# Kernel tuning notes

Measured on AMD Instinct MI355X. Metric: run time of the kernel, lower is better.

Reference implementation:

```python
import jax, jax.numpy as jnp
import numpy as np

FFT_LEN = 256
WIN_LEN = 768
FRM_LEN = 128
PPF_TAP = WIN_LEN // FFT_LEN  # 6
SCALE = -256.0
GROUP_DELAY = 648  # module uses group_delay = -648
B, C, S, T = 8, 2, FFT_LEN // 2 + 1, 4096


def _make_lpf(win_len):
    # firwin(win_len, 0.5, window='hann', scale=False) equivalent
    n = np.arange(win_len, dtype=np.float64)
    w = 0.5 - 0.5 * np.cos(2.0 * np.pi * n / (win_len - 1))
    h = w * np.sinc(0.5 * (n - (win_len - 1) / 2.0))
    return jnp.asarray(h, dtype=jnp.float32)


def setup_inputs() -> dict:
    key = jax.random.key(0)
    k1, k2 = jax.random.split(key)
    spectrum_real = jax.random.normal(k1, (B, C, S, T), dtype=jnp.float32)
    spectrum_imag = jax.random.normal(k2, (B, C, S, T), dtype=jnp.float32)
    lpf_coef = _make_lpf(WIN_LEN)
    return {"spectrum_real": spectrum_real, "spectrum_imag": spectrum_imag, "lpf_coef": lpf_coef}


def reference(spectrum_real, spectrum_imag, lpf_coef):
    # spectrum: (B, C, S, T) complex; per-frame irfft over subbands
    spec = jnp.swapaxes(spectrum_real + 1j * spectrum_imag, -1, -2)  # (B,C,T,S)
    fftout = jnp.fft.irfft(spec, n=FFT_LEN, axis=-1)                 # (B,C,T,FFT_LEN)
    rev = fftout[..., ::-1]                                          # comp_in[fft_len-j-1]
    v = jnp.tile(rev, (1, 1, 1, PPF_TAP)) * lpf_coef                 # (B,C,T,WIN_LEN)
    b, c, t, _ = v.shape
    num_samples = t * FRM_LEN
    # overlap-add: frame t contributes v[t] at offset t*FRM_LEN (shifting buffer recurrence)
    idx = jnp.arange(t)[:, None] * FRM_LEN + jnp.arange(WIN_LEN)[None, :]  # (T, WIN_LEN)
    y = jnp.zeros((b, c, num_samples + WIN_LEN), dtype=v.dtype)
    y = y.at[..., idx].add(v)[..., :num_samples]
    y = y * (FRM_LEN * SCALE)
    # circular shift by group delay, then trim the wrapped tail
    y = jnp.roll(y, -GROUP_DELAY, axis=-1)[..., :-GROUP_DELAY]
    return y
```

## Files before the change

### kernel.cpp

```cpp
#include <hip/hip_runtime.h>
#include <hip/hip_bf16.h>
#include <math.h>

#define NBINS   129
#define NFFT    256
#define WINL    768
#define TFRAMES 4096
#define OUTL    523640
#define SHIFT   648
#define WSEG    26
#define CHUNK   (WSEG * 128)
#define NCHUNK  ((OUTL + CHUNK - 1) / CHUNK)
#define FF      32

#define KDIM    288
#define KROW    296
#define GROW    268
#define WBYTES  (16 * 9 * 64 * 16)
#define GBYTES  ((size_t)16 * TFRAMES * 256 * 2)
#define NSTG    17

typedef __attribute__((ext_vector_type(8))) short bf16x8;
typedef __attribute__((ext_vector_type(4))) float f32x4;

static __device__ __forceinline__ ushort f2bf(float x) {
    union { float f; unsigned u; } v; v.f = x;
    unsigned r = v.u + 0x7FFFu + ((v.u >> 16) & 1u);
    return (ushort)(r >> 16);
}

__global__ void build_w_kernel(ushort* __restrict__ wp)
{
    const int gid  = blockIdx.x * 256 + threadIdx.x;
    const int lane = gid & 63;
    const int mtks = gid >> 6;
    const int ks   = mtks % 9;
    const int mt   = mtks / 9;
    const int m    = mt * 16 + (lane & 15);
    const int kb   = ks * 32 + ((lane >> 4) << 3);

    ushort o[8];
    #pragma unroll
    for (int e = 0; e < 8; ++e) {
        const int kap = kb + e;
        float val = 0.f;
        if (kap < 258) {
            const int k = kap >> 1;
            float s, c;
            sincospif((float)(k * (m + 1)) * (1.0f / 128.0f), &s, &c);
            if (kap & 1)  val = (k >= 1 && k <= 127) ? s * (2.0f / 256.0f) : 0.f;
            else          val = (k == 0 || k == 128) ? c * (1.0f / 256.0f)
                                                     : c * (2.0f / 256.0f);
        }
        o[e] = f2bf(val);
    }
    int4 pk;
    pk.x = o[0] | (o[1] << 16); pk.y = o[2] | (o[3] << 16);
    pk.z = o[4] | (o[5] << 16); pk.w = o[6] | (o[7] << 16);
    ((int4*)wp)[gid] = pk;
}

__global__ __launch_bounds__(256, 4)
void pfb_dft_kernel(const float* __restrict__ gre, const float* __restrict__ gim,
                    const ushort* __restrict__ wp, ushort* __restrict__ Gg)
{
    __shared__ ushort s_bufu[FF * KROW];
    ushort* s_Bu = s_bufu;
    ushort (*s_G)[NFFT] = (ushort (*)[NFFT])s_bufu;

    const int t0  = blockIdx.x * FF;
    const int bc  = blockIdx.y;
    const int tid = threadIdx.x;
    const size_t specBase = (size_t)bc * NBINS * TFRAMES;

    float vr[NSTG], vi[NSTG];
    #pragma unroll
    for (int r = 0; r < NSTG; ++r) {
        const int idx = tid + r * 256;
        float a = 0.f, b = 0.f;
        if (idx < NBINS * FF) {
            const int k = idx >> 5, f = idx & 31;
            const size_t g = specBase + (size_t)k * TFRAMES + (size_t)(t0 + f);
            a = gre[g]; b = gim[g];
        }
        vr[r] = a; vi[r] = b;
    }
    #pragma unroll
    for (int r = 0; r < NSTG; ++r) {
        const int idx = tid + r * 256;
        if (idx < NBINS * FF) {
            const int k = idx >> 5, f = idx & 31;
            __hip_bfloat162 p = __float22bfloat162_rn(make_float2(vr[r], vi[r]));
            *(__hip_bfloat162*)&s_Bu[f * KROW + 2 * k] = p;
        }
    }
    for (int idx = tid; idx < FF * (KROW - 258); idx += 256) {
        const int f = idx / (KROW - 258), r = idx - f * (KROW - 258);
        s_Bu[f * KROW + 258 + r] = 0;
    }
    __syncthreads();

    const int lane = tid & 63;
    const int wid  = tid >> 6;
    const int brow = lane & 15;
    const int kgrp = (lane >> 4) << 3;

    bf16x8 bfrag[2][9];
    #pragma unroll
    for (int nt = 0; nt < 2; ++nt)
        #pragma unroll
        for (int ks = 0; ks < 9; ++ks)
            bfrag[nt][ks] = *(const bf16x8*)&s_Bu[(nt * 16 + brow) * KROW + ks * 32 + kgrp];

    f32x4 acc[4][2];
    #pragma unroll
    for (int mi = 0; mi < 4; ++mi)
        #pragma unroll
        for (int nt = 0; nt < 2; ++nt)
            acc[mi][nt] = (f32x4){0.f, 0.f, 0.f, 0.f};

    #pragma unroll 1
    for (int mi = 0; mi < 4; ++mi) {
        const ushort* wbase = wp + ((size_t)((wid * 4 + mi) * 9) * 64 + lane) * 8;
        #pragma unroll
        for (int ks = 0; ks < 9; ++ks) {
            const bf16x8 aw = *(const bf16x8*)(wbase + ks * 512);
            acc[mi][0] = __builtin_amdgcn_mfma_f32_16x16x32_bf16(aw, bfrag[0][ks], acc[mi][0], 0, 0, 0);
            acc[mi][1] = __builtin_amdgcn_mfma_f32_16x16x32_bf16(aw, bfrag[1][ks], acc[mi][1], 0, 0, 0);
        }
    }
    __syncthreads();

    #pragma unroll
    for (int mi = 0; mi < 4; ++mi) {
        const int m0 = (wid * 4 + mi) * 16 + ((lane >> 4) << 2);
        #pragma unroll
        for (int nt = 0; nt < 2; ++nt) {
            const int f = nt * 16 + brow;
            __hip_bfloat162 lo = __float22bfloat162_rn(make_float2(acc[mi][nt].x, acc[mi][nt].y));
            __hip_bfloat162 hi = __float22bfloat162_rn(make_float2(acc[mi][nt].z, acc[mi][nt].w));
            uint2 pk; pk.x = *(unsigned*)&lo; pk.y = *(unsigned*)&hi;
            *(uint2*)&s_G[f][m0] = pk;
        }
    }
    __syncthreads();

    ushort* gout = Gg + ((size_t)bc * TFRAMES + t0) * NFFT;
    #pragma unroll
    for (int j = 0; j < 4; ++j) {
        const int c   = tid + j * 256;
        const int row = c >> 5;
        const int col = (c & 31) * 8;
        *(bf16x8*)&gout[c * 8] = *(const bf16x8*)&s_G[row][col];
    }
}

__global__ __launch_bounds__(256, 8)
void pfb_oa_kernel(const ushort* __restrict__ Gg, const float* __restrict__ glpf,
                   float* __restrict__ out)
{
    const int tid = threadIdx.x;
    const int bc  = blockIdx.y;
    const int i0  = blockIdx.x * 2048 + tid;

    const int s0 = i0 + SHIFT;
    const int b  = s0 & 127;
    float lw[6];
    #pragma unroll
    for (int p = 0; p < 6; ++p) lw[p] = glpf[(p << 7) + b];

    const ushort* Gb = Gg + (size_t)bc * TFRAMES * NFFT;
    const size_t outBase = (size_t)bc * OUTL;

    #pragma unroll
    for (int j = 0; j < 8; ++j) {
        const int i = i0 + j * 256;
        if (i < OUTL) {
            const int a = (i + SHIFT) >> 7;
            const ushort* gp = Gb + (size_t)a * NFFT + b;
            float sum = 0.f;
            #pragma unroll
            for (int p = 0; p < 6; ++p) {
                union { unsigned u_; float f; } g;
                g.u_ = ((unsigned)gp[-(p << 8) + ((p & 1) << 7)]) << 16;
                sum += lw[p] * g.f;
            }
            out[outBase + i] = sum * (-32768.0f);
        }
    }
}

__global__ __launch_bounds__(256, 4)
void pfb_mfma_kernel(const float* __restrict__ gre, const float* __restrict__ gim,
                     const float* __restrict__ glpf, const ushort* __restrict__ wp,
                     float* __restrict__ out)
{
    __shared__ ushort s_bufu[FF * KROW];
    __shared__ float  s_lpf[WINL];
    ushort* s_Bu = s_bufu;
    ushort (*s_G)[GROW] = (ushort (*)[GROW])s_bufu;

    const int q   = blockIdx.x;
    const int bc  = blockIdx.y;
    const int tid = threadIdx.x;
    const int t0  = WSEG * q;
    const size_t specBase = (size_t)bc * NBINS * TFRAMES;

    for (int idx = tid; idx < WINL; idx += 256) s_lpf[idx] = glpf[idx];

    float vr[NSTG], vi[NSTG];
    #pragma unroll
    for (int r = 0; r < NSTG; ++r) {
        const int idx = tid + r * 256;
        const int k = idx >> 5, f = idx & 31;
        const int t = t0 + f;
        const bool ok = (idx < NBINS * FF) && (t < TFRAMES);
        float a = 0.f, bb = 0.f;
        if (ok) {
            const size_t g = specBase + (size_t)k * TFRAMES + (size_t)t;
            a = gre[g]; bb = gim[g];
        }
        vr[r] = a; vi[r] = bb;
    }
    #pragma unroll
    for (int r = 0; r < NSTG; ++r) {
        const int idx = tid + r * 256;
        if (idx < NBINS * FF) {
            const int k = idx >> 5, f = idx & 31;
            __hip_bfloat162 p = __float22bfloat162_rn(make_float2(vr[r], vi[r]));
            *(__hip_bfloat162*)&s_Bu[f * KROW + 2 * k] = p;
        }
    }
    for (int idx = tid; idx < FF * (KROW - 258); idx += 256) {
        const int f = idx / (KROW - 258), r = idx - f * (KROW - 258);
        s_Bu[f * KROW + 258 + r] = 0;
    }
    __syncthreads();

    const int lane = tid & 63;
    const int wid  = tid >> 6;
    const int brow = lane & 15;
    const int kgrp = (lane >> 4) << 3;

    bf16x8 bfrag[2][9];
    #pragma unroll
    for (int nt = 0; nt < 2; ++nt)
        #pragma unroll
        for (int ks = 0; ks < 9; ++ks)
            bfrag[nt][ks] = *(const bf16x8*)&s_Bu[(nt * 16 + brow) * KROW + ks * 32 + kgrp];

    f32x4 acc[4][2];
    #pragma unroll
    for (int mi = 0; mi < 4; ++mi)
        #pragma unroll
        for (int nt = 0; nt < 2; ++nt)
            acc[mi][nt] = (f32x4){0.f, 0.f, 0.f, 0.f};

    #pragma unroll 1
    for (int mi = 0; mi < 4; ++mi) {
        const ushort* wbase = wp + ((size_t)((wid * 4 + mi) * 9) * 64 + lane) * 8;
        #pragma unroll
        for (int ks = 0; ks < 9; ++ks) {
            const bf16x8 aw = *(const bf16x8*)(wbase + ks * 512);
            acc[mi][0] = __builtin_amdgcn_mfma_f32_16x16x32_bf16(aw, bfrag[0][ks], acc[mi][0], 0, 0, 0);
            acc[mi][1] = __builtin_amdgcn_mfma_f32_16x16x32_bf16(aw, bfrag[1][ks], acc[mi][1], 0, 0, 0);
        }
    }
    __syncthreads();

    #pragma unroll
    for (int mi = 0; mi < 4; ++mi) {
        const int m0 = (wid * 4 + mi) * 16 + ((lane >> 4) << 2);
        #pragma unroll
        for (int nt = 0; nt < 2; ++nt) {
            const int f = nt * 16 + brow;
            __hip_bfloat162 lo = __float22bfloat162_rn(make_float2(acc[mi][nt].x, acc[mi][nt].y));
            __hip_bfloat162 hi = __float22bfloat162_rn(make_float2(acc[mi][nt].z, acc[mi][nt].w));
            uint2 pk; pk.x = *(unsigned*)&lo; pk.y = *(unsigned*)&hi;
            *(uint2*)&s_G[f][m0] = pk;
        }
    }
    __syncthreads();

    const size_t outBase = (size_t)bc * OUTL;
    const int i0 = q * CHUNK;
    #pragma unroll 1
    for (int r = 0; r < 13; ++r) {
        const int i = i0 + r * 256 + tid;
        const int s = i + SHIFT;
        const int tlo = (s - 640) >> 7;
        int thi = s >> 7;
        if (thi > t0 + FF - 1) thi = t0 + FF - 1;
        if (thi > TFRAMES - 1) thi = TFRAMES - 1;
        float sum = 0.f;
        #pragma unroll
        for (int u = 0; u < 6; ++u) {
            const int t  = tlo + u;
            int jj = s - (t << 7);
            if (jj < 0) jj = 0;
            const float w = s_lpf[jj];
            union { unsigned u_; float f; } g;
            g.u_ = ((unsigned)s_G[t - t0][jj & 255]) << 16;
            sum += (t <= thi) ? w * g.f : 0.f;
        }
        if (i < OUTL) out[outBase + i] = sum * (-32768.0f);
    }
}

extern "C" void kernel_launch(void* const* d_in, const int* in_sizes, int n_in,
                              void* d_out, int out_size, void* d_ws, size_t ws_size,
                              hipStream_t stream)
{
    const float* gre  = (const float*)d_in[0];
    const float* gim  = (const float*)d_in[1];
    const float* glpf = (const float*)d_in[2];
    float* out = (float*)d_out;

    if (ws_size >= (size_t)WBYTES + GBYTES) {
        ushort* wp = (ushort*)d_ws;
        ushort* Gg = (ushort*)((char*)d_ws + WBYTES);
        build_w_kernel<<<36, 256, 0, stream>>>(wp);
        dim3 gridA(TFRAMES / FF, 16);
        pfb_dft_kernel<<<gridA, 256, 0, stream>>>(gre, gim, wp, Gg);
        dim3 gridB((OUTL + 2047) / 2048, 16);
        pfb_oa_kernel<<<gridB, 256, 0, stream>>>(Gg, glpf, out);
    } else if (ws_size >= (size_t)WBYTES) {
        ushort* wp = (ushort*)d_ws;
        build_w_kernel<<<36, 256, 0, stream>>>(wp);
        dim3 grid(NCHUNK, 16);
        pfb_mfma_kernel<<<grid, 256, 0, stream>>>(gre, gim, glpf, wp, out);
    }
}
```

Baseline: 62.62 us.

## Stream B fragments per k-step, write DFT output directly, and pair-vectorize overlap-add

```diff
diff --git a/kernel.cpp b/kernel.cpp
--- a/kernel.cpp
+++ b/kernel.cpp
@@ -7,6 +7,7 @@
 #define WINL    768
 #define TFRAMES 4096
 #define OUTL    523640
+#define NPAIRS  (OUTL / 2)
 #define SHIFT   648
 #define WSEG    26
 #define CHUNK   (WSEG * 128)
@@ -60,13 +61,11 @@
     ((int4*)wp)[gid] = pk;
 }
 
-__global__ __launch_bounds__(256, 4)
+__global__ __launch_bounds__(256, 6)
 void pfb_dft_kernel(const float* __restrict__ gre, const float* __restrict__ gim,
                     const ushort* __restrict__ wp, ushort* __restrict__ Gg)
 {
-    __shared__ ushort s_bufu[FF * KROW];
-    ushort* s_Bu = s_bufu;
-    ushort (*s_G)[NFFT] = (ushort (*)[NFFT])s_bufu;
+    __shared__ ushort s_Bu[FF * KROW];
 
     const int t0  = blockIdx.x * FF;
     const int bc  = blockIdx.y;
@@ -105,13 +104,6 @@
     const int brow = lane & 15;
     const int kgrp = (lane >> 4) << 3;
 
-    bf16x8 bfrag[2][9];
-    #pragma unroll
-    for (int nt = 0; nt < 2; ++nt)
-        #pragma unroll
-        for (int ks = 0; ks < 9; ++ks)
-            bfrag[nt][ks] = *(const bf16x8*)&s_Bu[(nt * 16 + brow) * KROW + ks * 32 + kgrp];
-
     f32x4 acc[4][2];
     #pragma unroll
     for (int mi = 0; mi < 4; ++mi)
@@ -119,18 +111,20 @@
         for (int nt = 0; nt < 2; ++nt)
             acc[mi][nt] = (f32x4){0.f, 0.f, 0.f, 0.f};
 
-    #pragma unroll 1
-    for (int mi = 0; mi < 4; ++mi) {
-        const ushort* wbase = wp + ((size_t)((wid * 4 + mi) * 9) * 64 + lane) * 8;
-        #pragma unroll
-        for (int ks = 0; ks < 9; ++ks) {
-            const bf16x8 aw = *(const bf16x8*)(wbase + ks * 512);
-            acc[mi][0] = __builtin_amdgcn_mfma_f32_16x16x32_bf16(aw, bfrag[0][ks], acc[mi][0], 0, 0, 0);
-            acc[mi][1] = __builtin_amdgcn_mfma_f32_16x16x32_bf16(aw, bfrag[1][ks], acc[mi][1], 0, 0, 0);
-        }
-    }
-    __syncthreads();
-
+    const ushort* wbase0 = wp + ((size_t)(wid * 4) * 9 * 64 + (size_t)lane) * 8;
+    #pragma unroll
+    for (int ks = 0; ks < 9; ++ks) {
+        const bf16x8 b0 = *(const bf16x8*)&s_Bu[brow * KROW + ks * 32 + kgrp];
+        const bf16x8 b1 = *(const bf16x8*)&s_Bu[(16 + brow) * KROW + ks * 32 + kgrp];
+        #pragma unroll
+        for (int mi = 0; mi < 4; ++mi) {
+            const bf16x8 aw = *(const bf16x8*)(wbase0 + mi * 4608 + ks * 512);
+            acc[mi][0] = __builtin_amdgcn_mfma_f32_16x16x32_bf16(aw, b0, acc[mi][0], 0, 0, 0);
+            acc[mi][1] = __builtin_amdgcn_mfma_f32_16x16x32_bf16(aw, b1, acc[mi][1], 0, 0, 0);
+        }
+    }
+
+    ushort* gout = Gg + ((size_t)bc * TFRAMES + t0) * NFFT;
     #pragma unroll
     for (int mi = 0; mi < 4; ++mi) {
         const int m0 = (wid * 4 + mi) * 16 + ((lane >> 4) << 2);
@@ -140,18 +134,8 @@
             __hip_bfloat162 lo = __float22bfloat162_rn(make_float2(acc[mi][nt].x, acc[mi][nt].y));
             __hip_bfloat162 hi = __float22bfloat162_rn(make_float2(acc[mi][nt].z, acc[mi][nt].w));
             uint2 pk; pk.x = *(unsigned*)&lo; pk.y = *(unsigned*)&hi;
-            *(uint2*)&s_G[f][m0] = pk;
-        }
-    }
-    __syncthreads();
-
-    ushort* gout = Gg + ((size_t)bc * TFRAMES + t0) * NFFT;
-    #pragma unroll
-    for (int j = 0; j < 4; ++j) {
-        const int c   = tid + j * 256;
-        const int row = c >> 5;
-        const int col = (c & 31) * 8;
-        *(bf16x8*)&gout[c * 8] = *(const bf16x8*)&s_G[row][col];
+            *(uint2*)&gout[f * NFFT + m0] = pk;
+        }
     }
 }
 
@@ -161,31 +145,34 @@
 {
     const int tid = threadIdx.x;
     const int bc  = blockIdx.y;
-    const int i0  = blockIdx.x * 2048 + tid;
-
-    const int s0 = i0 + SHIFT;
-    const int b  = s0 & 127;
-    float lw[6];
-    #pragma unroll
-    for (int p = 0; p < 6; ++p) lw[p] = glpf[(p << 7) + b];
+    const int g0  = blockIdx.x * 1024 + tid;
+
+    const int b = (2 * g0 + SHIFT) & 127;
+    float2 lw[6];
+    #pragma unroll
+    for (int p = 0; p < 6; ++p) lw[p] = *(const float2*)&glpf[(p << 7) + b];
 
     const ushort* Gb = Gg + (size_t)bc * TFRAMES * NFFT;
     const size_t outBase = (size_t)bc * OUTL;
 
     #pragma unroll
-    for (int j = 0; j < 8; ++j) {
-        const int i = i0 + j * 256;
-        if (i < OUTL) {
-            const int a = (i + SHIFT) >> 7;
-            const ushort* gp = Gb + (size_t)a * NFFT + b;
-            float sum = 0.f;
-            #pragma unroll
-            for (int p = 0; p < 6; ++p) {
-                union { unsigned u_; float f; } g;
-                g.u_ = ((unsigned)gp[-(p << 8) + ((p & 1) << 7)]) << 16;
-                sum += lw[p] * g.f;
-            }
-            out[outBase + i] = sum * (-32768.0f);
+    for (int j = 0; j < 4; ++j) {
+        const int g = g0 + j * 256;
+        int a = (2 * g + SHIFT) >> 7;
+        if (a > TFRAMES - 1) a = TFRAMES - 1;
+        float sx = 0.f, sy = 0.f;
+        #pragma unroll
+        for (int p = 0; p < 6; ++p) {
+            const unsigned pr = *(const unsigned*)&Gb[(size_t)(a - p) * NFFT + b + ((p & 1) << 7)];
+            union { unsigned u; float f; } glo, ghi;
+            glo.u = pr << 16;
+            ghi.u = pr & 0xFFFF0000u;
+            sx += lw[p].x * glo.f;
+            sy += lw[p].y * ghi.f;
+        }
+        if (g < NPAIRS) {
+            float2 o; o.x = sx * (-32768.0f); o.y = sy * (-32768.0f);
+            *(float2*)&out[outBase + 2 * g] = o;
         }
     }
 }
@@ -322,7 +309,7 @@
         build_w_kernel<<<36, 256, 0, stream>>>(wp);
         dim3 gridA(TFRAMES / FF, 16);
         pfb_dft_kernel<<<gridA, 256, 0, stream>>>(gre, gim, wp, Gg);
-        dim3 gridB((OUTL + 2047) / 2048, 16);
+        dim3 gridB((NPAIRS + 1023) / 1024, 16);
         pfb_oa_kernel<<<gridB, 256, 0, stream>>>(Gg, glpf, out);
     } else if (ws_size >= (size_t)WBYTES) {
         ushort* wp = (ushort*)d_ws;
```

Result: faster. 56.36 us (-10.0%).
